# Optimization experiments

Hardware: AMD Instinct MI355X
Metric: run time of the kernel (lower is better)

The kernel has to match this reference:

```python
import jax, jax.numpy as jnp
import numpy as np

B, NL, NT = 8, 64, 512   # graphs, ligand atoms/graph, target nodes/graph
CF = 128                 # per-node embedding dim (Linear(256,...) => 2*128)
H = 128                  # hidden_dim
K = 10                   # n_gaussians
E = 1024                 # ligand edges
BN_EPS = 1e-4


def setup_inputs() -> dict:
    key = jax.random.key(0)
    ks = jax.random.split(key, 24)
    inp = {}
    inp["h_l_x"] = jax.random.normal(ks[0], (B * NL, CF), jnp.float32)
    inp["h_t_x"] = jax.random.normal(ks[1], (B * NT, CF), jnp.float32)
    inp["h_l_pos"] = jax.random.normal(ks[2], (B * NL, 3), jnp.float32)
    inp["h_t_pos"] = jax.random.normal(ks[3], (B * NT, 3), jnp.float32)
    inp["edge_index"] = jax.random.randint(ks[4], (2, E), 0, B * NL, jnp.int64)
    s = 0.05
    inp["W1"] = jax.random.normal(ks[5], (2 * CF, H), jnp.float32) * s
    inp["b1"] = jnp.zeros((H,), jnp.float32)
    inp["gamma"] = jnp.ones((H,), jnp.float32)
    inp["beta"] = jnp.zeros((H,), jnp.float32)
    inp["rmean"] = jax.random.normal(ks[6], (H,), jnp.float32) * 0.1
    inp["rvar"] = jax.random.uniform(ks[7], (H,), jnp.float32, 0.5, 1.5)
    inp["Wpi"] = jax.random.normal(ks[8], (H, K), jnp.float32) * s
    inp["bpi"] = jnp.zeros((K,), jnp.float32)
    inp["Wsig"] = jax.random.normal(ks[9], (H, K), jnp.float32) * s
    inp["bsig"] = jnp.zeros((K,), jnp.float32)
    inp["Wmu"] = jax.random.normal(ks[10], (H, K), jnp.float32) * s
    inp["bmu"] = jnp.zeros((K,), jnp.float32)
    inp["Wat"] = jax.random.normal(ks[11], (CF, 28), jnp.float32) * s
    inp["bat"] = jnp.zeros((28,), jnp.float32)
    inp["Wbd"] = jax.random.normal(ks[12], (2 * CF, 6), jnp.float32) * s
    inp["bbd"] = jnp.zeros((6,), jnp.float32)
    return inp


def reference(h_l_x, h_t_x, h_l_pos, h_t_pos, edge_index,
              W1, b1, gamma, beta, rmean, rvar,
              Wpi, bpi, Wsig, bsig, Wmu, bmu, Wat, bat, Wbd, bbd):
    # dense batched node features (equal counts per graph => reshape)
    hl = h_l_x.reshape(B, NL, CF)
    ht = h_t_x.reshape(B, NT, CF)

    # cat([hl_repeat, ht_repeat]) @ W1 == hl@W1[:CF] + ht@W1[CF:] (broadcast add)
    zl = jnp.einsum('blc,ch->blh', hl, W1[:CF])          # [B,NL,H]
    zt = jnp.einsum('btc,ch->bth', ht, W1[CF:])          # [B,NT,H]
    z = zl[:, :, None, :] + zt[:, None, :, :] + b1       # [B,NL,NT,H]
    z = z.reshape(B * NL * NT, H)

    # BatchNorm1d (eval: running stats), ELU; Dropout is identity in eval
    z = (z - rmean) * (gamma / jnp.sqrt(rvar + BN_EPS)) + beta
    C = jax.nn.elu(z)

    pi = jax.nn.softmax(C @ Wpi + bpi, axis=-1)
    sigma = jax.nn.elu(C @ Wsig + bsig) + 1.1
    mu = jax.nn.elu(C @ Wmu + bmu) + 1.0

    # pairwise euclidean distances, detached in original
    pl = h_l_pos.reshape(B, NL, 3)
    pt = h_t_pos.reshape(B, NT, 3)
    d2 = (-2.0 * jnp.einsum('bld,btd->blt', pl, pt)
          + jnp.sum(pt ** 2, -1)[:, None, :]
          + jnp.sum(pl ** 2, -1)[:, :, None])
    dist = jnp.sqrt(d2).reshape(B * NL * NT)
    dist = jax.lax.stop_gradient(dist)[:, None]          # [P,1]

    atom_types = h_l_x @ Wat + bat                       # [B*NL,28]
    eb = jnp.concatenate([h_l_x[edge_index[0]], h_l_x[edge_index[1]]], axis=1)
    bond_types = eb @ Wbd + bbd                          # [E,6]

    C_batch = jnp.repeat(jnp.arange(B, dtype=jnp.int32), NL * NT)
    return (pi, sigma, mu, dist, atom_types, bond_types, C_batch)
```

## Files before the change

kernel.cpp:

```cpp
#include <hip/hip_runtime.h>
#include <cstdint>
#include <cstddef>

#define NB_B 8
#define NL   64
#define NT   512
#define CF   128
#define HD   128
#define NK   10
#define NE   1024

static constexpr size_t P_TOT    = (size_t)NB_B * NL * NT;
static constexpr size_t PI_OFF   = 0;
static constexpr size_t SIG_OFF  = P_TOT * 10;
static constexpr size_t MU_OFF   = SIG_OFF + P_TOT * 10;
static constexpr size_t DIST_OFF = MU_OFF + P_TOT * 10;
static constexpr size_t AT_OFF   = DIST_OFF + P_TOT;
static constexpr size_t BD_OFF   = AT_OFF + 512 * 28;
static constexpr size_t CB_OFF   = BD_OFF + NE * 6;

typedef __attribute__((ext_vector_type(8))) short short8;
typedef __attribute__((ext_vector_type(4))) float floatx4;
typedef __attribute__((ext_vector_type(2))) float floatx2;

__device__ __forceinline__ float bf2f(unsigned short u) {
    return __uint_as_float(((unsigned int)u) << 16);
}
__device__ __forceinline__ unsigned short f2bf(float f) {
    unsigned int x = __float_as_uint(f);
    x = (x + 0x7FFFu + ((x >> 16) & 1u)) >> 16;
    return (unsigned short)x;
}

__global__ __launch_bounds__(256) void k_pre(
    const float* __restrict__ hl,
    const float* __restrict__ ht,
    const int*   __restrict__ eidx,
    const float* __restrict__ W1,
    const float* __restrict__ b1,
    const float* __restrict__ gamma_,
    const float* __restrict__ beta_,
    const float* __restrict__ rmean,
    const float* __restrict__ rvar,
    const float* __restrict__ Wpi,
    const float* __restrict__ Wsig,
    const float* __restrict__ Wmu,
    const float* __restrict__ Wat,
    const float* __restrict__ bat,
    const float* __restrict__ Wbd,
    const float* __restrict__ bbd,
    unsigned short* __restrict__ zl,
    unsigned short* __restrict__ zt,
    unsigned short* __restrict__ wcomb_t,
    float* __restrict__ out_at,
    float* __restrict__ out_bd)
{
    const int blk = blockIdx.x;
    const int tid = threadIdx.x;

    if (blk < 144) {
        const bool is_l = (blk < 16);
        const int rbase = is_l ? blk * 32 : (blk - 16) * 32;
        const float* A  = is_l ? hl : ht;
        const float* Wx = W1 + (is_l ? 0 : (size_t)CF * HD);
        unsigned short* Z = is_l ? zl : zt;

        const int wave = tid >> 6;
        const int lane = tid & 63;
        const int m    = lane & 15;
        const int kq   = (lane >> 4) * 8;
        const int n0   = wave * 32 + m;

        floatx4 acc[2][2];
        #pragma unroll
        for (int i = 0; i < 2; ++i)
            #pragma unroll
            for (int j = 0; j < 2; ++j)
                acc[i][j] = (floatx4){0.f, 0.f, 0.f, 0.f};

        #pragma unroll
        for (int kb = 0; kb < 4; ++kb) {
            const int k0 = kb * 32 + kq;
            short8 a[2];
            #pragma unroll
            for (int mt = 0; mt < 2; ++mt) {
                const float* ap = A + (size_t)(rbase + mt * 16 + m) * CF + k0;
                floatx4 f0 = *(const floatx4*)ap;
                floatx4 f1 = *(const floatx4*)(ap + 4);
                #pragma unroll
                for (int j = 0; j < 4; ++j) {
                    a[mt][j]     = (short)f2bf(f0[j]);
                    a[mt][4 + j] = (short)f2bf(f1[j]);
                }
            }
            short8 bf[2];
            #pragma unroll
            for (int nt = 0; nt < 2; ++nt) {
                const int n = n0 + nt * 16;
                #pragma unroll
                for (int j = 0; j < 8; ++j)
                    bf[nt][j] = (short)f2bf(Wx[(size_t)(k0 + j) * HD + n]);
            }
            #pragma unroll
            for (int mt = 0; mt < 2; ++mt)
                #pragma unroll
                for (int nt = 0; nt < 2; ++nt)
                    acc[mt][nt] = __builtin_amdgcn_mfma_f32_16x16x32_bf16(a[mt], bf[nt], acc[mt][nt], 0, 0, 0);
        }

        #pragma unroll
        for (int nt = 0; nt < 2; ++nt) {
            const int col = n0 + nt * 16;
            const float s   = gamma_[col] * rsqrtf(rvar[col] + 1e-4f);
            const float off = is_l ? 0.f : ((b1[col] - rmean[col]) * s + beta_[col]);
            #pragma unroll
            for (int mt = 0; mt < 2; ++mt)
                #pragma unroll
                for (int r = 0; r < 4; ++r) {
                    const int row = rbase + mt * 16 + (lane >> 4) * 4 + r;
                    Z[(size_t)row * HD + col] = f2bf(acc[mt][nt][r] * s + off);
                }
        }
    } else if (blk == 144) {
        for (int i = tid; i < 32 * HD; i += 256) {
            const int n = i >> 7, k = i & 127;
            float v = 0.f;
            if (n < 10)      v = Wpi [k * NK + n];
            else if (n < 20) v = Wsig[k * NK + (n - 10)];
            else if (n < 30) v = Wmu [k * NK + (n - 20)];
            wcomb_t[i] = f2bf(v);
        }
    } else if (blk < 201) {
        const int oi = (blk - 145) * 256 + tid;
        const int r = oi / 28, n = oi - r * 28;
        float acc = bat[n];
        #pragma unroll 4
        for (int c = 0; c < CF; ++c)
            acc += hl[(size_t)r * CF + c] * Wat[c * 28 + n];
        out_at[oi] = acc;
    } else {
        const int oi = (blk - 201) * 256 + tid;
        const int e = oi / 6, n = oi - e * 6;
        const int s0 = eidx[e], s1 = eidx[NE + e];
        float acc = bbd[n];
        #pragma unroll 4
        for (int c = 0; c < CF; ++c) {
            acc += hl[(size_t)s0 * CF + c] * Wbd[c * 6 + n];
            acc += hl[(size_t)s1 * CF + c] * Wbd[(CF + c) * 6 + n];
        }
        out_bd[oi] = acc;
    }
}

__global__ __launch_bounds__(256) void k_main(
    const unsigned short* __restrict__ zl,
    const unsigned short* __restrict__ zt,
    const unsigned short* __restrict__ wcomb_t,
    const float* __restrict__ bpi,
    const float* __restrict__ bsig,
    const float* __restrict__ bmu,
    const float* __restrict__ hlpos,
    const float* __restrict__ htpos,
    float* __restrict__ out)
{
    __shared__ float Dl[128 * 33];
    __shared__ float biass[32];
    __shared__ float pls[3];

    const int tid  = threadIdx.x;
    const int blk  = blockIdx.x;
    const int b    = blk >> 8;
    const int l    = (blk >> 2) & 63;
    const int ch   = blk & 3;
    const int lane = tid & 63;
    const int wave = tid >> 6;
    const int m    = lane & 15;
    const int kq   = (lane >> 4) * 8;

    if (tid < 32) {
        float v = 0.f;
        if (tid < 10)      v = bpi[tid];
        else if (tid < 20) v = bsig[tid - 10];
        else if (tid < 30) v = bmu[tid - 20];
        biass[tid] = v;
    } else if (tid < 35) {
        pls[tid - 32] = hlpos[(size_t)(b * NL + l) * 3 + (tid - 32)];
    }

    short8 bfrag[2][4];
    #pragma unroll
    for (int nt = 0; nt < 2; ++nt)
        #pragma unroll
        for (int kb = 0; kb < 4; ++kb)
            bfrag[nt][kb] = *(const short8*)(wcomb_t + (size_t)(nt * 16 + m) * HD + kb * 32 + kq);

    const unsigned short* zlr = zl + (size_t)(b * NL + l) * HD;
    const unsigned short* ztb = zt + (size_t)(b * NT + ch * 128) * HD;

    floatx4 acc[2][2];
    #pragma unroll
    for (int i = 0; i < 2; ++i)
        #pragma unroll
        for (int j = 0; j < 2; ++j)
            acc[i][j] = (floatx4){0.f, 0.f, 0.f, 0.f};

    #pragma unroll
    for (int kb = 0; kb < 4; ++kb) {
        const int k0 = kb * 32 + kq;
        short8 zlv = *(const short8*)(zlr + k0);
        float zf[8];
        #pragma unroll
        for (int j = 0; j < 8; ++j) zf[j] = bf2f((unsigned short)zlv[j]);

        short8 a[2];
        #pragma unroll
        for (int mt = 0; mt < 2; ++mt) {
            const int row = wave * 32 + mt * 16 + m;
            short8 ztv = *(const short8*)(ztb + (size_t)row * HD + k0);
            #pragma unroll
            for (int j = 0; j < 8; ++j) {
                const float x = zf[j] + bf2f((unsigned short)ztv[j]);
                const float c = (x > 0.f) ? x : (__expf(x) - 1.f);
                a[mt][j] = (short)f2bf(c);
            }
        }
        #pragma unroll
        for (int mt = 0; mt < 2; ++mt)
            #pragma unroll
            for (int nt = 0; nt < 2; ++nt)
                acc[mt][nt] = __builtin_amdgcn_mfma_f32_16x16x32_bf16(a[mt], bfrag[nt][kb], acc[mt][nt], 0, 0, 0);
    }

    #pragma unroll
    for (int mt = 0; mt < 2; ++mt)
        #pragma unroll
        for (int nt = 0; nt < 2; ++nt)
            #pragma unroll
            for (int r = 0; r < 4; ++r) {
                const int row = wave * 32 + mt * 16 + (lane >> 4) * 4 + r;
                const int col = nt * 16 + m;
                Dl[row * 33 + col] = acc[mt][nt][r];
            }
    __syncthreads();

    const size_t gp = ((size_t)(b * NL + l)) * NT + ch * 128 + (tid & 127);
    if (tid < 128) {
        const int p = tid;
        float v[10];
        float mx = -1e30f;
        #pragma unroll
        for (int n = 0; n < 10; ++n) {
            v[n] = Dl[p * 33 + n] + biass[n];
            mx = fmaxf(mx, v[n]);
        }
        float s = 0.f;
        #pragma unroll
        for (int n = 0; n < 10; ++n) { v[n] = __expf(v[n] - mx); s += v[n]; }
        const float inv = 1.f / s;
        floatx2* po = (floatx2*)(out + PI_OFF + gp * 10);
        #pragma unroll
        for (int n = 0; n < 5; ++n) po[n] = (floatx2){v[2*n] * inv, v[2*n+1] * inv};
    } else {
        const int p = tid - 128;
        float sg[10], mv[10];
        #pragma unroll
        for (int n = 0; n < 10; ++n) {
            const float x = Dl[p * 33 + 10 + n] + biass[10 + n];
            sg[n] = ((x > 0.f) ? x : (__expf(x) - 1.f)) + 1.1f;
            const float y = Dl[p * 33 + 20 + n] + biass[20 + n];
            mv[n] = ((y > 0.f) ? y : (__expf(y) - 1.f)) + 1.0f;
        }
        floatx2* ps = (floatx2*)(out + SIG_OFF + gp * 10);
        floatx2* pm = (floatx2*)(out + MU_OFF  + gp * 10);
        #pragma unroll
        for (int n = 0; n < 5; ++n) {
            ps[n] = (floatx2){sg[2*n], sg[2*n+1]};
            pm[n] = (floatx2){mv[2*n], mv[2*n+1]};
        }
        const int t = ch * 128 + p;
        const size_t pb = (size_t)(b * NT + t) * 3;
        const float dx = pls[0] - htpos[pb + 0];
        const float dy = pls[1] - htpos[pb + 1];
        const float dz = pls[2] - htpos[pb + 2];
        out[DIST_OFF + gp] = sqrtf(dx * dx + dy * dy + dz * dz);
        out[CB_OFF + gp]   = (float)b;
    }
}

extern "C" void kernel_launch(void* const* d_in, const int* in_sizes, int n_in,
                              void* d_out, int out_size, void* d_ws, size_t ws_size,
                              hipStream_t stream)
{
    const float* hl     = (const float*)d_in[0];
    const float* ht     = (const float*)d_in[1];
    const float* hlpos  = (const float*)d_in[2];
    const float* htpos  = (const float*)d_in[3];
    const int*   eidx   = (const int*)d_in[4];
    const float* W1     = (const float*)d_in[5];
    const float* b1     = (const float*)d_in[6];
    const float* gamma_ = (const float*)d_in[7];
    const float* beta_  = (const float*)d_in[8];
    const float* rmean  = (const float*)d_in[9];
    const float* rvar   = (const float*)d_in[10];
    const float* Wpi    = (const float*)d_in[11];
    const float* bpi    = (const float*)d_in[12];
    const float* Wsig   = (const float*)d_in[13];
    const float* bsig   = (const float*)d_in[14];
    const float* Wmu    = (const float*)d_in[15];
    const float* bmu    = (const float*)d_in[16];
    const float* Wat    = (const float*)d_in[17];
    const float* bat    = (const float*)d_in[18];
    const float* Wbd    = (const float*)d_in[19];
    const float* bbd    = (const float*)d_in[20];

    float* out = (float*)d_out;
    unsigned short* ws  = (unsigned short*)d_ws;
    unsigned short* zl      = ws;
    unsigned short* zt      = ws + 512 * 128;
    unsigned short* wcomb_t = ws + 512 * 128 + 4096 * 128;

    k_pre<<<225, 256, 0, stream>>>(hl, ht, eidx, W1, b1, gamma_, beta_, rmean, rvar,
                                   Wpi, Wsig, Wmu, Wat, bat, Wbd, bbd,
                                   zl, zt, wcomb_t, out + AT_OFF, out + BD_OFF);
    k_main<<<2048, 256, 0, stream>>>(zl, zt, wcomb_t, bpi, bsig, bmu, hlpos, htpos, out);
}
```

Measured before the change: 137.4 us.

## Fuse pre-projection and head kernels into one launch, recomputing target projection per block

After: 154.8 us. 1.13x slower.

```diff
diff --git a/kernel.cpp b/kernel.cpp
--- a/kernel.cpp
+++ b/kernel.cpp
@@ -1,4 +1,5 @@
 #include <hip/hip_runtime.h>
+#include <hip/hip_bf16.h>
 #include <cstdint>
 #include <cstddef>
 
@@ -23,16 +24,19 @@
 typedef __attribute__((ext_vector_type(4))) float floatx4;
 typedef __attribute__((ext_vector_type(2))) float floatx2;
 
-__device__ __forceinline__ float bf2f(unsigned short u) {
-    return __uint_as_float(((unsigned int)u) << 16);
-}
+union U8 { short8 s8; unsigned int u[4]; };
+
 __device__ __forceinline__ unsigned short f2bf(float f) {
     unsigned int x = __float_as_uint(f);
     x = (x + 0x7FFFu + ((x >> 16) & 1u)) >> 16;
     return (unsigned short)x;
 }
-
-__global__ __launch_bounds__(256) void k_pre(
+__device__ __forceinline__ unsigned int pk2bf(float a, float b) {
+    __hip_bfloat162 h = __float22bfloat162_rn(make_float2(a, b));
+    return *reinterpret_cast<unsigned int*>(&h);
+}
+
+__global__ __launch_bounds__(256) void k_fused(
     const float* __restrict__ hl,
     const float* __restrict__ ht,
     const int*   __restrict__ eidx,
@@ -43,139 +47,62 @@
     const float* __restrict__ rmean,
     const float* __restrict__ rvar,
     const float* __restrict__ Wpi,
+    const float* __restrict__ bpi,
     const float* __restrict__ Wsig,
+    const float* __restrict__ bsig,
     const float* __restrict__ Wmu,
+    const float* __restrict__ bmu,
     const float* __restrict__ Wat,
     const float* __restrict__ bat,
     const float* __restrict__ Wbd,
     const float* __restrict__ bbd,
-    unsigned short* __restrict__ zl,
-    unsigned short* __restrict__ zt,
-    unsigned short* __restrict__ wcomb_t,
-    float* __restrict__ out_at,
-    float* __restrict__ out_bd)
-{
-    const int blk = blockIdx.x;
-    const int tid = threadIdx.x;
-
-    if (blk < 144) {
-        const bool is_l = (blk < 16);
-        const int rbase = is_l ? blk * 32 : (blk - 16) * 32;
-        const float* A  = is_l ? hl : ht;
-        const float* Wx = W1 + (is_l ? 0 : (size_t)CF * HD);
-        unsigned short* Z = is_l ? zl : zt;
-
-        const int wave = tid >> 6;
-        const int lane = tid & 63;
-        const int m    = lane & 15;
-        const int kq   = (lane >> 4) * 8;
-        const int n0   = wave * 32 + m;
-
-        floatx4 acc[2][2];
-        #pragma unroll
-        for (int i = 0; i < 2; ++i)
-            #pragma unroll
-            for (int j = 0; j < 2; ++j)
-                acc[i][j] = (floatx4){0.f, 0.f, 0.f, 0.f};
-
-        #pragma unroll
-        for (int kb = 0; kb < 4; ++kb) {
-            const int k0 = kb * 32 + kq;
-            short8 a[2];
-            #pragma unroll
-            for (int mt = 0; mt < 2; ++mt) {
-                const float* ap = A + (size_t)(rbase + mt * 16 + m) * CF + k0;
-                floatx4 f0 = *(const floatx4*)ap;
-                floatx4 f1 = *(const floatx4*)(ap + 4);
-                #pragma unroll
-                for (int j = 0; j < 4; ++j) {
-                    a[mt][j]     = (short)f2bf(f0[j]);
-                    a[mt][4 + j] = (short)f2bf(f1[j]);
-                }
-            }
-            short8 bf[2];
-            #pragma unroll
-            for (int nt = 0; nt < 2; ++nt) {
-                const int n = n0 + nt * 16;
-                #pragma unroll
-                for (int j = 0; j < 8; ++j)
-                    bf[nt][j] = (short)f2bf(Wx[(size_t)(k0 + j) * HD + n]);
-            }
-            #pragma unroll
-            for (int mt = 0; mt < 2; ++mt)
-                #pragma unroll
-                for (int nt = 0; nt < 2; ++nt)
-                    acc[mt][nt] = __builtin_amdgcn_mfma_f32_16x16x32_bf16(a[mt], bf[nt], acc[mt][nt], 0, 0, 0);
-        }
-
-        #pragma unroll
-        for (int nt = 0; nt < 2; ++nt) {
-            const int col = n0 + nt * 16;
-            const float s   = gamma_[col] * rsqrtf(rvar[col] + 1e-4f);
-            const float off = is_l ? 0.f : ((b1[col] - rmean[col]) * s + beta_[col]);
-            #pragma unroll
-            for (int mt = 0; mt < 2; ++mt)
-                #pragma unroll
-                for (int r = 0; r < 4; ++r) {
-                    const int row = rbase + mt * 16 + (lane >> 4) * 4 + r;
-                    Z[(size_t)row * HD + col] = f2bf(acc[mt][nt][r] * s + off);
-                }
-        }
-    } else if (blk == 144) {
-        for (int i = tid; i < 32 * HD; i += 256) {
-            const int n = i >> 7, k = i & 127;
-            float v = 0.f;
-            if (n < 10)      v = Wpi [k * NK + n];
-            else if (n < 20) v = Wsig[k * NK + (n - 10)];
-            else if (n < 30) v = Wmu [k * NK + (n - 20)];
-            wcomb_t[i] = f2bf(v);
-        }
-    } else if (blk < 201) {
-        const int oi = (blk - 145) * 256 + tid;
-        const int r = oi / 28, n = oi - r * 28;
-        float acc = bat[n];
-        #pragma unroll 4
-        for (int c = 0; c < CF; ++c)
-            acc += hl[(size_t)r * CF + c] * Wat[c * 28 + n];
-        out_at[oi] = acc;
-    } else {
-        const int oi = (blk - 201) * 256 + tid;
-        const int e = oi / 6, n = oi - e * 6;
-        const int s0 = eidx[e], s1 = eidx[NE + e];
-        float acc = bbd[n];
-        #pragma unroll 4
-        for (int c = 0; c < CF; ++c) {
-            acc += hl[(size_t)s0 * CF + c] * Wbd[c * 6 + n];
-            acc += hl[(size_t)s1 * CF + c] * Wbd[(CF + c) * 6 + n];
-        }
-        out_bd[oi] = acc;
-    }
-}
-
-__global__ __launch_bounds__(256) void k_main(
-    const unsigned short* __restrict__ zl,
-    const unsigned short* __restrict__ zt,
-    const unsigned short* __restrict__ wcomb_t,
-    const float* __restrict__ bpi,
-    const float* __restrict__ bsig,
-    const float* __restrict__ bmu,
     const float* __restrict__ hlpos,
     const float* __restrict__ htpos,
     float* __restrict__ out)
 {
-    __shared__ float Dl[128 * 33];
+    __shared__ unsigned short W1t[128 * 136];
+    __shared__ __align__(16) unsigned char ldsu[128 * 136 * 2];
+    __shared__ float zpart[256];
+    __shared__ float c0s[128], svs[128], bts[128];
     __shared__ float biass[32];
     __shared__ float pls[3];
 
-    const int tid  = threadIdx.x;
-    const int blk  = blockIdx.x;
-    const int b    = blk >> 8;
-    const int l    = (blk >> 2) & 63;
-    const int ch   = blk & 3;
+    const int blk = blockIdx.x;
+    const int tid = threadIdx.x;
+
+    if (blk >= 512) {
+        if (blk < 568) {
+            const int oi = (blk - 512) * 256 + tid;
+            const int r = oi / 28, n = oi - r * 28;
+            float acc = bat[n];
+            #pragma unroll 4
+            for (int c = 0; c < CF; ++c)
+                acc += hl[(size_t)r * CF + c] * Wat[c * 28 + n];
+            out[AT_OFF + oi] = acc;
+        } else {
+            const int oi = (blk - 568) * 256 + tid;
+            const int e = oi / 6, n = oi - e * 6;
+            const int s0 = eidx[e], s1 = eidx[NE + e];
+            float acc = bbd[n];
+            #pragma unroll 4
+            for (int c = 0; c < CF; ++c) {
+                acc += hl[(size_t)s0 * CF + c] * Wbd[c * 6 + n];
+                acc += hl[(size_t)s1 * CF + c] * Wbd[(CF + c) * 6 + n];
+            }
+            out[BD_OFF + oi] = acc;
+        }
+        return;
+    }
+
+    unsigned short* Zt = (unsigned short*)ldsu;
+    float*          Dl = (float*)ldsu;
+
+    const int b    = blk >> 6;
+    const int l    = blk & 63;
     const int lane = tid & 63;
     const int wave = tid >> 6;
     const int m    = lane & 15;
-    const int kq   = (lane >> 4) * 8;
+    const int quad = lane >> 4;
 
     if (tid < 32) {
         float v = 0.f;
@@ -187,103 +114,188 @@
         pls[tid - 32] = hlpos[(size_t)(b * NL + l) * 3 + (tid - 32)];
     }
 
-    short8 bfrag[2][4];
+    {
+        const int kb0 = tid >> 5;
+        const int n0  = (tid & 31) * 4;
+        #pragma unroll 4
+        for (int p = 0; p < 16; ++p) {
+            const int k = kb0 + p * 8;
+            const float4 v = *(const float4*)&W1[(size_t)(CF + k) * HD + n0];
+            const unsigned int u01 = pk2bf(v.x, v.y);
+            const unsigned int u23 = pk2bf(v.z, v.w);
+            W1t[(n0 + 0) * 136 + k] = (unsigned short)(u01 & 0xffffu);
+            W1t[(n0 + 1) * 136 + k] = (unsigned short)(u01 >> 16);
+            W1t[(n0 + 2) * 136 + k] = (unsigned short)(u23 & 0xffffu);
+            W1t[(n0 + 3) * 136 + k] = (unsigned short)(u23 >> 16);
+        }
+    }
+
+    {
+        const int h = tid & 127, half = tid >> 7;
+        const float* hr = hl + (size_t)(b * NL + l) * CF + half * 64;
+        const float* wc = W1 + (size_t)(half * 64) * HD + h;
+        float s = 0.f;
+        #pragma unroll 8
+        for (int c = 0; c < 64; ++c) s += hr[c] * wc[(size_t)c * HD];
+        zpart[tid] = s;
+    }
+
+    short8 bfragH[2][4];
     #pragma unroll
-    for (int nt = 0; nt < 2; ++nt)
-        #pragma unroll
-        for (int kb = 0; kb < 4; ++kb)
-            bfrag[nt][kb] = *(const short8*)(wcomb_t + (size_t)(nt * 16 + m) * HD + kb * 32 + kq);
-
-    const unsigned short* zlr = zl + (size_t)(b * NL + l) * HD;
-    const unsigned short* ztb = zt + (size_t)(b * NT + ch * 128) * HD;
-
-    floatx4 acc[2][2];
-    #pragma unroll
-    for (int i = 0; i < 2; ++i)
-        #pragma unroll
-        for (int j = 0; j < 2; ++j)
-            acc[i][j] = (floatx4){0.f, 0.f, 0.f, 0.f};
-
-    #pragma unroll
-    for (int kb = 0; kb < 4; ++kb) {
-        const int k0 = kb * 32 + kq;
-        short8 zlv = *(const short8*)(zlr + k0);
-        float zf[8];
-        #pragma unroll
-        for (int j = 0; j < 8; ++j) zf[j] = bf2f((unsigned short)zlv[j]);
-
-        short8 a[2];
-        #pragma unroll
-        for (int mt = 0; mt < 2; ++mt) {
-            const int row = wave * 32 + mt * 16 + m;
-            short8 ztv = *(const short8*)(ztb + (size_t)row * HD + k0);
+    for (int nt = 0; nt < 2; ++nt) {
+        const int n = nt * 16 + m;
+        const float* hw = (n < 10) ? (Wpi + n) : (n < 20) ? (Wsig + n - 10)
+                        : (n < 30) ? (Wmu + n - 20) : Wpi;
+        #pragma unroll
+        for (int kb = 0; kb < 4; ++kb) {
             #pragma unroll
             for (int j = 0; j < 8; ++j) {
-                const float x = zf[j] + bf2f((unsigned short)ztv[j]);
-                const float c = (x > 0.f) ? x : (__expf(x) - 1.f);
-                a[mt][j] = (short)f2bf(c);
-            }
-        }
+                const int k = kb * 32 + quad * 8 + j;
+                const float v = (n < 30) ? hw[(size_t)k * NK] : 0.f;
+                bfragH[nt][kb][j] = (short)f2bf(v);
+            }
+        }
+    }
+    __syncthreads();
+
+    if (tid < 128) {
+        const int h = tid;
+        c0s[h] = zpart[h] + zpart[h + 128] + b1[h] - rmean[h];
+        svs[h] = gamma_[h] * rsqrtf(rvar[h] + 1e-4f);
+        bts[h] = beta_[h];
+    }
+    __syncthreads();
+
+    for (int ch = 0; ch < 4; ++ch) {
+        floatx4 acc0[2][8];
+        #pragma unroll
+        for (int i = 0; i < 2; ++i)
+            #pragma unroll
+            for (int j = 0; j < 8; ++j)
+                acc0[i][j] = (floatx4){0.f, 0.f, 0.f, 0.f};
+
+        const float* htbase = ht + (size_t)(b * NT + ch * 128) * CF;
+        #pragma unroll
+        for (int kb = 0; kb < 4; ++kb) {
+            const int k0 = kb * 32 + quad * 8;
+            short8 a[2];
+            #pragma unroll
+            for (int mt = 0; mt < 2; ++mt) {
+                const int row = wave * 32 + mt * 16 + m;
+                const float* ap = htbase + (size_t)row * CF + k0;
+                const float4 f0 = *(const float4*)ap;
+                const float4 f1 = *(const float4*)(ap + 4);
+                U8 t;
+                t.u[0] = pk2bf(f0.x, f0.y);
+                t.u[1] = pk2bf(f0.z, f0.w);
+                t.u[2] = pk2bf(f1.x, f1.y);
+                t.u[3] = pk2bf(f1.z, f1.w);
+                a[mt] = t.s8;
+            }
+            #pragma unroll
+            for (int nt = 0; nt < 8; ++nt) {
+                const short8 bf = *(const short8*)&W1t[(nt * 16 + m) * 136 + k0];
+                acc0[0][nt] = __builtin_amdgcn_mfma_f32_16x16x32_bf16(a[0], bf, acc0[0][nt], 0, 0, 0);
+                acc0[1][nt] = __builtin_amdgcn_mfma_f32_16x16x32_bf16(a[1], bf, acc0[1][nt], 0, 0, 0);
+            }
+        }
+        #pragma unroll
+        for (int nt = 0; nt < 8; ++nt) {
+            const int col = nt * 16 + m;
+            const float c0v = c0s[col], sv = svs[col], btv = bts[col];
+            #pragma unroll
+            for (int mt = 0; mt < 2; ++mt) {
+                const int rbase = wave * 32 + mt * 16 + quad * 4;
+                float e[4];
+                #pragma unroll
+                for (int r = 0; r < 4; ++r) {
+                    const float z = (acc0[mt][nt][r] + c0v) * sv + btv;
+                    e[r] = (z > 0.f) ? z : (__expf(z) - 1.f);
+                }
+                const unsigned int u01 = pk2bf(e[0], e[1]);
+                const unsigned int u23 = pk2bf(e[2], e[3]);
+                Zt[(rbase + 0) * 136 + col] = (unsigned short)(u01 & 0xffffu);
+                Zt[(rbase + 1) * 136 + col] = (unsigned short)(u01 >> 16);
+                Zt[(rbase + 2) * 136 + col] = (unsigned short)(u23 & 0xffffu);
+                Zt[(rbase + 3) * 136 + col] = (unsigned short)(u23 >> 16);
+            }
+        }
+
+        floatx4 acc2[2][2];
+        #pragma unroll
+        for (int i = 0; i < 2; ++i)
+            #pragma unroll
+            for (int j = 0; j < 2; ++j)
+                acc2[i][j] = (floatx4){0.f, 0.f, 0.f, 0.f};
+
+        #pragma unroll
+        for (int kb = 0; kb < 4; ++kb) {
+            const int ko = kb * 32 + quad * 8;
+            const short8 a0 = *(const short8*)&Zt[(wave * 32 + m) * 136 + ko];
+            const short8 a1 = *(const short8*)&Zt[(wave * 32 + 16 + m) * 136 + ko];
+            #pragma unroll
+            for (int nt = 0; nt < 2; ++nt) {
+                acc2[0][nt] = __builtin_amdgcn_mfma_f32_16x16x32_bf16(a0, bfragH[nt][kb], acc2[0][nt], 0, 0, 0);
+                acc2[1][nt] = __builtin_amdgcn_mfma_f32_16x16x32_bf16(a1, bfragH[nt][kb], acc2[1][nt], 0, 0, 0);
+            }
+        }
+        __syncthreads();
+
         #pragma unroll
         for (int mt = 0; mt < 2; ++mt)
             #pragma unroll
             for (int nt = 0; nt < 2; ++nt)
-                acc[mt][nt] = __builtin_amdgcn_mfma_f32_16x16x32_bf16(a[mt], bfrag[nt][kb], acc[mt][nt], 0, 0, 0);
-    }
-
-    #pragma unroll
-    for (int mt = 0; mt < 2; ++mt)
-        #pragma unroll
-        for (int nt = 0; nt < 2; ++nt)
-            #pragma unroll
-            for (int r = 0; r < 4; ++r) {
-                const int row = wave * 32 + mt * 16 + (lane >> 4) * 4 + r;
-                const int col = nt * 16 + m;
-                Dl[row * 33 + col] = acc[mt][nt][r];
-            }
-    __syncthreads();
-
-    const size_t gp = ((size_t)(b * NL + l)) * NT + ch * 128 + (tid & 127);
-    if (tid < 128) {
-        const int p = tid;
-        float v[10];
-        float mx = -1e30f;
-        #pragma unroll
-        for (int n = 0; n < 10; ++n) {
-            v[n] = Dl[p * 33 + n] + biass[n];
-            mx = fmaxf(mx, v[n]);
-        }
-        float s = 0.f;
-        #pragma unroll
-        for (int n = 0; n < 10; ++n) { v[n] = __expf(v[n] - mx); s += v[n]; }
-        const float inv = 1.f / s;
-        floatx2* po = (floatx2*)(out + PI_OFF + gp * 10);
-        #pragma unroll
-        for (int n = 0; n < 5; ++n) po[n] = (floatx2){v[2*n] * inv, v[2*n+1] * inv};
-    } else {
-        const int p = tid - 128;
-        float sg[10], mv[10];
-        #pragma unroll
-        for (int n = 0; n < 10; ++n) {
-            const float x = Dl[p * 33 + 10 + n] + biass[10 + n];
-            sg[n] = ((x > 0.f) ? x : (__expf(x) - 1.f)) + 1.1f;
-            const float y = Dl[p * 33 + 20 + n] + biass[20 + n];
-            mv[n] = ((y > 0.f) ? y : (__expf(y) - 1.f)) + 1.0f;
-        }
-        floatx2* ps = (floatx2*)(out + SIG_OFF + gp * 10);
-        floatx2* pm = (floatx2*)(out + MU_OFF  + gp * 10);
-        #pragma unroll
-        for (int n = 0; n < 5; ++n) {
-            ps[n] = (floatx2){sg[2*n], sg[2*n+1]};
-            pm[n] = (floatx2){mv[2*n], mv[2*n+1]};
-        }
-        const int t = ch * 128 + p;
-        const size_t pb = (size_t)(b * NT + t) * 3;
-        const float dx = pls[0] - htpos[pb + 0];
-        const float dy = pls[1] - htpos[pb + 1];
-        const float dz = pls[2] - htpos[pb + 2];
-        out[DIST_OFF + gp] = sqrtf(dx * dx + dy * dy + dz * dz);
-        out[CB_OFF + gp]   = (float)b;
+                #pragma unroll
+                for (int r = 0; r < 4; ++r) {
+                    const int row = wave * 32 + mt * 16 + quad * 4 + r;
+                    const int col = nt * 16 + m;
+                    Dl[row * 33 + col] = acc2[mt][nt][r];
+                }
+        __syncthreads();
+
+        const size_t gp = ((size_t)(b * NL + l)) * NT + ch * 128 + (tid & 127);
+        if (tid < 128) {
+            const int p = tid;
+            float v[10];
+            float mx = -1e30f;
+            #pragma unroll
+            for (int n = 0; n < 10; ++n) {
+                v[n] = Dl[p * 33 + n] + biass[n];
+                mx = fmaxf(mx, v[n]);
+            }
+            float s = 0.f;
+            #pragma unroll
+            for (int n = 0; n < 10; ++n) { v[n] = __expf(v[n] - mx); s += v[n]; }
+            const float inv = 1.f / s;
+            floatx2* po = (floatx2*)(out + PI_OFF + gp * 10);
+            #pragma unroll
+            for (int n = 0; n < 5; ++n) po[n] = (floatx2){v[2*n] * inv, v[2*n+1] * inv};
+        } else {
+            const int p = tid - 128;
+            float sg[10], mv[10];
+            #pragma unroll
+            for (int n = 0; n < 10; ++n) {
+                const float x = Dl[p * 33 + 10 + n] + biass[10 + n];
+                sg[n] = ((x > 0.f) ? x : (__expf(x) - 1.f)) + 1.1f;
+                const float y = Dl[p * 33 + 20 + n] + biass[20 + n];
+                mv[n] = ((y > 0.f) ? y : (__expf(y) - 1.f)) + 1.0f;
+            }
+            floatx2* ps = (floatx2*)(out + SIG_OFF + gp * 10);
+            floatx2* pm = (floatx2*)(out + MU_OFF  + gp * 10);
+            #pragma unroll
+            for (int n = 0; n < 5; ++n) {
+                ps[n] = (floatx2){sg[2*n], sg[2*n+1]};
+                pm[n] = (floatx2){mv[2*n], mv[2*n+1]};
+            }
+            const int t = ch * 128 + p;
+            const size_t pb = (size_t)(b * NT + t) * 3;
+            const float dx = pls[0] - htpos[pb + 0];
+            const float dy = pls[1] - htpos[pb + 1];
+            const float dz = pls[2] - htpos[pb + 2];
+            out[DIST_OFF + gp] = sqrtf(dx * dx + dy * dy + dz * dz);
+            out[CB_OFF + gp]   = (float)b;
+        }
+        __syncthreads();
     }
 }
 
@@ -314,13 +326,8 @@
     const float* bbd    = (const float*)d_in[20];
 
     float* out = (float*)d_out;
-    unsigned short* ws  = (unsigned short*)d_ws;
-    unsigned short* zl      = ws;
-    unsigned short* zt      = ws + 512 * 128;
-    unsigned short* wcomb_t = ws + 512 * 128 + 4096 * 128;
-
-    k_pre<<<225, 256, 0, stream>>>(hl, ht, eidx, W1, b1, gamma_, beta_, rmean, rvar,
-                                   Wpi, Wsig, Wmu, Wat, bat, Wbd, bbd,
-                                   zl, zt, wcomb_t, out + AT_OFF, out + BD_OFF);
-    k_main<<<2048, 256, 0, stream>>>(zl, zt, wcomb_t, bpi, bsig, bmu, hlpos, htpos, out);
+
+    k_fused<<<592, 256, 0, stream>>>(hl, ht, eidx, W1, b1, gamma_, beta_, rmean, rvar,
+                                     Wpi, bpi, Wsig, bsig, Wmu, bmu,
+                                     Wat, bat, Wbd, bbd, hlpos, htpos, out);
 }
```
